# Kernel optimization log

Measured on AMD Instinct MI355X. Metric: run time of the kernel, lower is better.

Reference implementation:

```python
import jax, jax.numpy as jnp
import numpy as np

D_MODEL = 1024
N_LAYER = 4
D_INNER = 2048   # expand * d_model
D_STATE = 16
D_CONV = 4
DT_RANK = 64     # ceil(d_model / 16)
B, L = 2, 1024
EPS = 1e-5


def setup_inputs() -> dict:
    key = jax.random.key(0)
    ks = jax.random.split(key, 10)
    nl = N_LAYER
    def nrm(k, shape, s=0.02):
        return jax.random.normal(k, shape, jnp.float32) * s
    A_log = jnp.broadcast_to(jnp.log(jnp.arange(1, D_STATE + 1, dtype=jnp.float32)),
                             (nl, D_INNER, D_STATE)) + jnp.zeros((nl, D_INNER, D_STATE), jnp.float32)
    return {
        "hidden_states": jax.random.normal(ks[0], (B, L, D_MODEL), jnp.float32),
        "in_proj_w": nrm(ks[1], (nl, 2 * D_INNER, D_MODEL)),
        "conv_w": nrm(ks[2], (nl, D_INNER, D_CONV), 0.1),
        "conv_b": nrm(ks[3], (nl, D_INNER), 0.02),
        "x_proj_w": nrm(ks[4], (nl, DT_RANK + 2 * D_STATE, D_INNER)),
        "dt_proj_w": nrm(ks[5], (nl, D_INNER, DT_RANK), DT_RANK ** -0.5),
        "dt_proj_b": jnp.log(jnp.expm1(jax.random.uniform(ks[6], (nl, D_INNER), jnp.float32, 1e-3, 0.1))),
        "A_log": A_log,
        "D": jnp.ones((nl, D_INNER), jnp.float32),
        "out_proj_w": nrm(ks[7], (nl, D_MODEL, D_INNER)),
        "norm_w": jnp.ones((nl, D_MODEL), jnp.float32),
        "norm_b": jnp.zeros((nl, D_MODEL), jnp.float32),
        "normf_w": jnp.ones((D_MODEL,), jnp.float32),
        "normf_b": jnp.zeros((D_MODEL,), jnp.float32),
    }


def _layernorm(x, w, b):
    mu = x.mean(-1, keepdims=True)
    var = ((x - mu) ** 2).mean(-1, keepdims=True)
    return (x - mu) * jax.lax.rsqrt(var + EPS) * w + b


def _mamba(h, iw, cw, cb, xw, dw, db, Alog, Dp, ow):
    Bn, Ln, _ = h.shape
    xz = jnp.einsum('bld,ed->ble', h, iw)          # [B,L,2*d_inner]
    x, z = jnp.split(xz, 2, axis=-1)
    # depthwise causal conv1d over time, kernel size D_CONV
    xp = jnp.pad(x, ((0, 0), (D_CONV - 1, 0), (0, 0)))
    xc = sum(xp[:, k:k + Ln, :] * cw[:, k] for k in range(D_CONV)) + cb
    x = jax.nn.silu(xc)
    dbl = jnp.einsum('bld,ed->ble', x, xw)         # [B,L,dt_rank+2*d_state]
    dt = dbl[..., :DT_RANK]
    Bm = dbl[..., DT_RANK:DT_RANK + D_STATE]
    Cm = dbl[..., DT_RANK + D_STATE:]
    dt = jax.nn.softplus(jnp.einsum('blr,dr->bld', dt, dw) + db)  # [B,L,d_inner]
    A = -jnp.exp(Alog)                              # [d_inner,d_state]

    def step(hc, inp):
        dt_t, B_t, C_t, x_t = inp                   # [B,d],[B,s],[B,s],[B,d]
        dA = jnp.exp(dt_t[:, :, None] * A)
        hc = hc * dA + (dt_t * x_t)[:, :, None] * B_t[:, None, :]
        y_t = jnp.einsum('bds,bs->bd', hc, C_t)
        return hc, y_t

    h0 = jnp.zeros((Bn, D_INNER, D_STATE), x.dtype)
    xs = (dt.transpose(1, 0, 2), Bm.transpose(1, 0, 2),
          Cm.transpose(1, 0, 2), x.transpose(1, 0, 2))
    _, ys = jax.lax.scan(step, h0, xs)              # ys: [L,B,d_inner]
    y = ys.transpose(1, 0, 2) + x * Dp
    y = y * jax.nn.silu(z)
    return jnp.einsum('bld,ed->ble', y, ow)


def reference(hidden_states, in_proj_w, conv_w, conv_b, x_proj_w, dt_proj_w,
              dt_proj_b, A_log, D, out_proj_w, norm_w, norm_b, normf_w, normf_b):
    hs = hidden_states
    residual = None
    for i in range(N_LAYER):
        residual = hs if residual is None else hs + residual
        hs = _layernorm(residual, norm_w[i], norm_b[i])
        hs = _mamba(hs, in_proj_w[i], conv_w[i], conv_b[i], x_proj_w[i],
                    dt_proj_w[i], dt_proj_b[i], A_log[i], D[i], out_proj_w[i])
    residual = hs + residual
    return _layernorm(residual, normf_w, normf_b)
```

## Files before the change

kernel.cpp:

```cpp
#include <hip/hip_runtime.h>
#include <math.h>

#define D_MODEL 1024
#define D_INNER 2048
#define D_STATE 16
#define D_CONV  4
#define DT_RANK 64
#define NB      2
#define LSEQ    1024
#define NROWS   (NB * LSEQ)
#define LN_EPS  1e-5f
#define N_LAYER 4
#define NCHUNK  32
#define TCH     (LSEQ / NCHUNK)

__device__ inline unsigned bfbits(float f) {
    unsigned u = __float_as_uint(f);
    return (u + 0x7fffu + ((u >> 16) & 1u)) >> 16;
}

#define GLOAD_LDS16(gp, lp) \
    __builtin_amdgcn_global_load_lds( \
        (const __attribute__((address_space(1))) void*)(gp), \
        (__attribute__((address_space(3))) void*)(lp), 16, 0, 0)

__device__ inline float wave_sum(float s) {
    #pragma unroll
    for (int m = 1; m < 64; m <<= 1) s += __shfl_xor(s, m, 64);
    return s;
}

__device__ inline void add_ln_body(int row, int tid,
                                   const float* __restrict__ add,
                                   float* __restrict__ residual,
                                   const float* __restrict__ w, const float* __restrict__ b,
                                   void* __restrict__ out, int first, int bf16out,
                                   float* red)
{
    size_t base = (size_t)row * D_MODEL + tid * 4;

    float4 v = *(const float4*)(add + base);
    if (!first) {
        float4 r = *(const float4*)(residual + base);
        v.x += r.x; v.y += r.y; v.z += r.z; v.w += r.w;
    }
    *(float4*)(residual + base) = v;

    float s = v.x + v.y + v.z + v.w;
    s = wave_sum(s);
    if ((tid & 63) == 0) red[tid >> 6] = s;
    __syncthreads();
    float mu = (red[0] + red[1] + red[2] + red[3]) * (1.0f / D_MODEL);

    float dx = v.x - mu, dy = v.y - mu, dz = v.z - mu, dw2 = v.w - mu;
    float s2 = dx*dx + dy*dy + dz*dz + dw2*dw2;
    s2 = wave_sum(s2);
    if ((tid & 63) == 0) red[4 + (tid >> 6)] = s2;
    __syncthreads();
    float var = (red[4] + red[5] + red[6] + red[7]) * (1.0f / D_MODEL);
    float rs = rsqrtf(var + LN_EPS);

    float4 wv = *(const float4*)(w + tid * 4);
    float4 bv = *(const float4*)(b + tid * 4);
    float4 o;
    o.x = dx  * rs * wv.x + bv.x;
    o.y = dy  * rs * wv.y + bv.y;
    o.z = dz  * rs * wv.z + bv.z;
    o.w = dw2 * rs * wv.w + bv.w;
    if (bf16out) {
        ushort4 ov;
        ov.x = (unsigned short)bfbits(o.x);
        ov.y = (unsigned short)bfbits(o.y);
        ov.z = (unsigned short)bfbits(o.z);
        ov.w = (unsigned short)bfbits(o.w);
        *(ushort4*)((unsigned short*)out + base) = ov;
    } else {
        *(float4*)((float*)out + base) = o;
    }
}

__global__ __launch_bounds__(256)
void add_ln_kernel(const float* __restrict__ add, float* __restrict__ residual,
                   const float* __restrict__ w, const float* __restrict__ b,
                   void* __restrict__ out, int first, int bf16out)
{
    __shared__ float red[8];
    add_ln_body(blockIdx.x, threadIdx.x, add, residual, w, b, out, first, bf16out, red);
}

__global__ __launch_bounds__(256)
void f32_to_bf16_kernel(const float* __restrict__ src, unsigned short* __restrict__ dst)
{
    int i = blockIdx.x * 256 + threadIdx.x;
    float4 v = *(const float4*)(src + (size_t)i * 4);
    ushort4 o;
    o.x = (unsigned short)bfbits(v.x);
    o.y = (unsigned short)bfbits(v.y);
    o.z = (unsigned short)bfbits(v.z);
    o.w = (unsigned short)bfbits(v.w);
    *(ushort4*)(dst + (size_t)i * 4) = o;
}

__device__ inline void hl_split4(float4 v, ushort4* h4, ushort4* l4)
{
    ushort4 h, l;
    float f;
    h.x = (unsigned short)bfbits(v.x); f = __uint_as_float((unsigned)h.x << 16); l.x = (unsigned short)bfbits(v.x - f);
    h.y = (unsigned short)bfbits(v.y); f = __uint_as_float((unsigned)h.y << 16); l.y = (unsigned short)bfbits(v.y - f);
    h.z = (unsigned short)bfbits(v.z); f = __uint_as_float((unsigned)h.z << 16); l.z = (unsigned short)bfbits(v.z - f);
    h.w = (unsigned short)bfbits(v.w); f = __uint_as_float((unsigned)h.w << 16); l.w = (unsigned short)bfbits(v.w - f);
    *h4 = h; *l4 = l;
}

__global__ __launch_bounds__(256)
void lnprep_kernel(const float* __restrict__ add, float* __restrict__ residual,
                   const float* __restrict__ w, const float* __restrict__ b,
                   unsigned short* __restrict__ ln_out, int first,
                   const float* __restrict__ iw, unsigned short* __restrict__ wbuf_in,
                   const float* __restrict__ xw, unsigned short* __restrict__ xwh,
                   unsigned short* __restrict__ xwl,
                   const float* __restrict__ dw, unsigned short* __restrict__ dwh,
                   unsigned short* __restrict__ dwl,
                   float* __restrict__ dbl)
{
    __shared__ float red[8];
    int b0 = blockIdx.x;
    int tid = threadIdx.x;
    if (b0 < 2048) {
        add_ln_body(b0, tid, add, residual, w, b, ln_out, first, 1, red);
    } else if (b0 < 6144) {
        int i = (b0 - 2048) * 256 + tid;
        float4 v = *(const float4*)(iw + (size_t)i * 4);
        ushort4 o;
        o.x = (unsigned short)bfbits(v.x);
        o.y = (unsigned short)bfbits(v.y);
        o.z = (unsigned short)bfbits(v.z);
        o.w = (unsigned short)bfbits(v.w);
        *(ushort4*)(wbuf_in + (size_t)i * 4) = o;
    } else if (b0 < 6336) {
        int i = (b0 - 6144) * 256 + tid;
        float4 v = *(const float4*)(xw + (size_t)i * 4);
        hl_split4(v, (ushort4*)(xwh + (size_t)i * 4), (ushort4*)(xwl + (size_t)i * 4));
    } else if (b0 < 6464) {
        int i = (b0 - 6336) * 256 + tid;
        float4 v = *(const float4*)(dw + (size_t)i * 4);
        hl_split4(v, (ushort4*)(dwh + (size_t)i * 4), (ushort4*)(dwl + (size_t)i * 4));
    } else {
        int i = (b0 - 6464) * 256 + tid;
        *(float4*)(dbl + (size_t)i * 4) = make_float4(0.f, 0.f, 0.f, 0.f);
    }
}

using bf16x8 = __attribute__((ext_vector_type(8))) short;
using f32x4  = __attribute__((ext_vector_type(4))) float;

#define BBM 128
#define BBN 128
#define BBK 64

__global__ __launch_bounds__(256)
void gemm_bf16_nt(const unsigned short* __restrict__ A, const unsigned short* __restrict__ Bw,
                  float* __restrict__ C, int M, int N, int K)
{
    __shared__ unsigned short As[BBM * BBK];
    __shared__ unsigned short Bs[BBN * BBK];

    int tid = threadIdx.x;
    int m0 = blockIdx.y * BBM, n0 = blockIdx.x * BBN;
    int lane = tid & 63, w = tid >> 6;
    int wm = (w >> 1) * 64, wn = (w & 1) * 64;
    int lm = lane & 15, q = lane >> 4;

    int lrow8 = lane >> 3;
    int scol  = ((lane & 7) ^ lrow8) * 8;

    f32x4 acc[4][4] = {};

    for (int k0 = 0; k0 < K; k0 += BBK) {
        #pragma unroll
        for (int j = 0; j < 4; ++j) {
            int rbase = w * 32 + j * 8;
            GLOAD_LDS16(A + (size_t)(m0 + rbase + lrow8) * K + k0 + scol,
                        &As[rbase * BBK]);
        }
        #pragma unroll
        for (int j = 0; j < 4; ++j) {
            int rbase = w * 32 + j * 8;
            GLOAD_LDS16(Bw + (size_t)(n0 + rbase + lrow8) * K + k0 + scol,
                        &Bs[rbase * BBK]);
        }
        __syncthreads();
        #pragma unroll
        for (int kk = 0; kk < BBK; kk += 32) {
            bf16x8 af[4], bf[4];
            #pragma unroll
            for (int i = 0; i < 4; ++i) {
                int row = wm + i * 16 + lm;
                int col = (kk + q * 8) ^ ((row & 7) << 3);
                af[i] = *(const bf16x8*)&As[row * BBK + col];
            }
            #pragma unroll
            for (int j = 0; j < 4; ++j) {
                int row = wn + j * 16 + lm;
                int col = (kk + q * 8) ^ ((row & 7) << 3);
                bf[j] = *(const bf16x8*)&Bs[row * BBK + col];
            }
            #pragma unroll
            for (int i = 0; i < 4; ++i)
                #pragma unroll
                for (int j = 0; j < 4; ++j)
                    acc[i][j] = __builtin_amdgcn_mfma_f32_16x16x32_bf16(
                        af[i], bf[j], acc[i][j], 0, 0, 0);
        }
        __syncthreads();
    }

    #pragma unroll
    for (int i = 0; i < 4; ++i)
        #pragma unroll
        for (int j = 0; j < 4; ++j)
            #pragma unroll
            for (int r = 0; r < 4; ++r) {
                int row = m0 + wm + i * 16 + q * 4 + r;
                int col = n0 + wn + j * 16 + lm;
                C[(size_t)row * N + col] = acc[i][j][r];
            }
}

__global__ __launch_bounds__(256)
void xproj_hl(const unsigned short* __restrict__ Ah, const unsigned short* __restrict__ Al,
              const unsigned short* __restrict__ Bh, const unsigned short* __restrict__ Bl,
              float* __restrict__ C)
{
    int tid = threadIdx.x;
    int lane = tid & 63, w = tid >> 6;
    int lm = lane & 15, q = lane >> 4;
    int m0 = blockIdx.x * 32;
    int kb = blockIdx.y * 256;

    int wm = (w & 1) * 16;
    int wn = (w >> 1) * 48;

    size_t arow = (size_t)(m0 + wm + lm) * 2048;

    f32x4 acc[3] = {};

    #pragma unroll 2
    for (int kc = 0; kc < 8; ++kc) {
        int k = kb + kc * 32 + q * 8;
        bf16x8 ah = *(const bf16x8*)&Ah[arow + k];
        bf16x8 al = *(const bf16x8*)&Al[arow + k];
        #pragma unroll
        for (int j = 0; j < 3; ++j) {
            size_t brow = (size_t)(wn + j * 16 + lm) * 2048;
            bf16x8 bh = *(const bf16x8*)&Bh[brow + k];
            bf16x8 bl = *(const bf16x8*)&Bl[brow + k];
            acc[j] = __builtin_amdgcn_mfma_f32_16x16x32_bf16(al, bh, acc[j], 0, 0, 0);
            acc[j] = __builtin_amdgcn_mfma_f32_16x16x32_bf16(ah, bl, acc[j], 0, 0, 0);
            acc[j] = __builtin_amdgcn_mfma_f32_16x16x32_bf16(ah, bh, acc[j], 0, 0, 0);
        }
    }

    #pragma unroll
    for (int j = 0; j < 3; ++j) {
        int col = wn + j * 16 + lm;
        #pragma unroll
        for (int r = 0; r < 4; ++r) {
            int row = m0 + wm + q * 4 + r;
            atomicAdd(&C[(size_t)row * 96 + col], acc[j][r]);
        }
    }
}

__global__ __launch_bounds__(256)
void dtproj_hl(const float* __restrict__ dbl,
               const unsigned short* __restrict__ Bh, const unsigned short* __restrict__ Bl,
               const float* __restrict__ bias, float* __restrict__ dtb)
{
    int tid = threadIdx.x;
    int lane = tid & 63, w = tid >> 6;
    int lm = lane & 15, q = lane >> 4;
    int n0 = blockIdx.x * 128;
    int m0 = blockIdx.y * 64;

    const float* arow = dbl + (size_t)(m0 + w * 16 + lm) * 96;

    f32x4 acc[8] = {};

    #pragma unroll
    for (int kc = 0; kc < 2; ++kc) {
        int k = kc * 32 + q * 8;
        float4 v0 = *(const float4*)(arow + k);
        float4 v1 = *(const float4*)(arow + k + 4);
        float vv[8] = {v0.x, v0.y, v0.z, v0.w, v1.x, v1.y, v1.z, v1.w};
        bf16x8 ah, al;
        #pragma unroll
        for (int s = 0; s < 8; ++s) {
            unsigned hb = bfbits(vv[s]);
            ah[s] = (short)hb;
            al[s] = (short)bfbits(vv[s] - __uint_as_float(hb << 16));
        }
        #pragma unroll
        for (int j = 0; j < 8; ++j) {
            size_t brow = (size_t)(n0 + j * 16 + lm) * 64;
            bf16x8 bh = *(const bf16x8*)&Bh[brow + k];
            bf16x8 bl = *(const bf16x8*)&Bl[brow + k];
            acc[j] = __builtin_amdgcn_mfma_f32_16x16x32_bf16(al, bh, acc[j], 0, 0, 0);
            acc[j] = __builtin_amdgcn_mfma_f32_16x16x32_bf16(ah, bl, acc[j], 0, 0, 0);
            acc[j] = __builtin_amdgcn_mfma_f32_16x16x32_bf16(ah, bh, acc[j], 0, 0, 0);
        }
    }

    #pragma unroll
    for (int j = 0; j < 8; ++j) {
        int col = n0 + j * 16 + lm;
        float bv = bias[col];
        #pragma unroll
        for (int r = 0; r < 4; ++r) {
            int row = m0 + w * 16 + q * 4 + r;
            float v = acc[j][r] + bv;
            v = (v > 20.f) ? v : log1pf(__expf(v));
            dtb[(size_t)row * D_INNER + col] = v;
        }
    }
}

__global__ __launch_bounds__(256)
void conv_silu_kernel(const float* __restrict__ xz, const float* __restrict__ cw,
                      const float* __restrict__ cb, float* __restrict__ xc,
                      unsigned short* __restrict__ xch, unsigned short* __restrict__ xcl)
{
    int idx = blockIdx.x * 256 + threadIdx.x;
    int d  = idx & (D_INNER - 1);
    int t  = (idx >> 11) & (LSEQ - 1);
    int bb = idx >> 21;

    const float* xcol = xz + (size_t)bb * LSEQ * 2 * D_INNER + d;
    float acc = cb[d];
    #pragma unroll
    for (int k = 0; k < D_CONV; ++k) {
        int tt = t + k - (D_CONV - 1);
        if (tt >= 0) acc += xcol[(size_t)tt * 2 * D_INNER] * cw[d * D_CONV + k];
    }
    acc = acc / (1.f + __expf(-acc));
    xc[idx] = acc;
    unsigned hb = bfbits(acc);
    xch[idx] = (unsigned short)hb;
    float hf = __uint_as_float(hb << 16);
    xcl[idx] = (unsigned short)bfbits(acc - hf);
}

#define UNPK4(dst, off, v) { dst[(off)+0]=(v).x; dst[(off)+1]=(v).y; \
                             dst[(off)+2]=(v).z; dst[(off)+3]=(v).w; }

__global__ __launch_bounds__(256)
void scan_pass1(const float* __restrict__ dtb, const float* __restrict__ xc,
                const float* __restrict__ dbl, const float* __restrict__ Alog,
                float* __restrict__ aPbuf, float* __restrict__ bAbuf)
{
    int tid  = threadIdx.x;
    int half = tid & 1;
    int blk  = blockIdx.x;
    int dg   = blk & 15;
    int c    = (blk >> 4) & (NCHUNK - 1);
    int bb   = blk >> 9;
    int d    = dg * 128 + (tid >> 1);

    float A[8];
    {
        const float* pA = Alog + (size_t)d * D_STATE + half * 8;
        float4 v0 = *(const float4*)pA;
        float4 v1 = *(const float4*)(pA + 4);
        A[0] = -__expf(v0.x); A[1] = -__expf(v0.y);
        A[2] = -__expf(v0.z); A[3] = -__expf(v0.w);
        A[4] = -__expf(v1.x); A[5] = -__expf(v1.y);
        A[6] = -__expf(v1.z); A[7] = -__expf(v1.w);
    }

    size_t rowbase = (size_t)bb * LSEQ + (size_t)c * TCH;
    const float* pdt = dtb + rowbase * D_INNER + d;
    const float* pxc = xc  + rowbase * D_INNER + d;
    const float* pbc = dbl + rowbase * 96 + DT_RANK + half * 8;

    float aP[8] = {1.f,1.f,1.f,1.f,1.f,1.f,1.f,1.f};
    float bA[8] = {0.f,0.f,0.f,0.f,0.f,0.f,0.f,0.f};

    float  dtE = pdt[0], xvE = pxc[0];
    float4 BE0 = *(const float4*)pbc;
    float4 BE1 = *(const float4*)(pbc + 4);
    float  dtO = pdt[D_INNER], xvO = pxc[D_INNER];
    float4 BO0 = *(const float4*)(pbc + 96);
    float4 BO1 = *(const float4*)(pbc + 96 + 4);

    const float* qdtE = pdt + 2 * D_INNER;
    const float* qdtO = pdt + 3 * D_INNER;
    const float* qxcE = pxc + 2 * D_INNER;
    const float* qxcO = pxc + 3 * D_INNER;
    const float* qbcE = pbc + 2 * 96;
    const float* qbcO = pbc + 3 * 96;

#define P1_STEP(DT, XV, B0, B1) { \
        float B[8]; UNPK4(B, 0, B0) UNPK4(B, 4, B1) \
        float dtx = (DT) * (XV); \
        _Pragma("unroll") \
        for (int s = 0; s < 8; ++s) { \
            float a = __expf((DT) * A[s]); \
            aP[s] *= a; \
            bA[s] = bA[s] * a + dtx * B[s]; \
        } }

    for (int t = 0; t < TCH - 4; t += 2) {
        float  dtEn = qdtE[0], xvEn = qxcE[0];
        float4 BE0n = *(const float4*)qbcE;
        float4 BE1n = *(const float4*)(qbcE + 4);
        float  dtOn = qdtO[0], xvOn = qxcO[0];
        float4 BO0n = *(const float4*)qbcO;
        float4 BO1n = *(const float4*)(qbcO + 4);
        qdtE += 2 * D_INNER; qdtO += 2 * D_INNER;
        qxcE += 2 * D_INNER; qxcO += 2 * D_INNER;
        qbcE += 192; qbcO += 192;

        P1_STEP(dtE, xvE, BE0, BE1)
        P1_STEP(dtO, xvO, BO0, BO1)

        dtE = dtEn; xvE = xvEn; BE0 = BE0n; BE1 = BE1n;
        dtO = dtOn; xvO = xvOn; BO0 = BO0n; BO1 = BO1n;
    }
    {
        float  dtEn = qdtE[0], xvEn = qxcE[0];
        float4 BE0n = *(const float4*)qbcE;
        float4 BE1n = *(const float4*)(qbcE + 4);
        float  dtOn = qdtO[0], xvOn = qxcO[0];
        float4 BO0n = *(const float4*)qbcO;
        float4 BO1n = *(const float4*)(qbcO + 4);

        P1_STEP(dtE, xvE, BE0, BE1)
        P1_STEP(dtO, xvO, BO0, BO1)

        dtE = dtEn; xvE = xvEn; BE0 = BE0n; BE1 = BE1n;
        dtO = dtOn; xvO = xvOn; BO0 = BO0n; BO1 = BO1n;
    }
    {
        P1_STEP(dtE, xvE, BE0, BE1)
        P1_STEP(dtO, xvO, BO0, BO1)
    }
#undef P1_STEP

    float* pa = aPbuf + ((size_t)(bb * NCHUNK + c) * D_INNER + d) * D_STATE + half * 8;
    float* pb = bAbuf + ((size_t)(bb * NCHUNK + c) * D_INNER + d) * D_STATE + half * 8;
    *(float4*)(pa + 0) = make_float4(aP[0], aP[1], aP[2], aP[3]);
    *(float4*)(pa + 4) = make_float4(aP[4], aP[5], aP[6], aP[7]);
    *(float4*)(pb + 0) = make_float4(bA[0], bA[1], bA[2], bA[3]);
    *(float4*)(pb + 4) = make_float4(bA[4], bA[5], bA[6], bA[7]);
}

__global__ __launch_bounds__(256)
void scan_pass2(const float* __restrict__ dtb, const float* __restrict__ xc,
                const float* __restrict__ dbl, const float* __restrict__ xz,
                const float* __restrict__ Alog, const float* __restrict__ Dp,
                const float* __restrict__ aPbuf, const float* __restrict__ bAbuf,
                unsigned short* __restrict__ y)
{
    int tid  = threadIdx.x;
    int half = tid & 1;
    int blk  = blockIdx.x;
    int dg   = blk & 15;
    int c    = (blk >> 4) & (NCHUNK - 1);
    int bb   = blk >> 9;
    int d    = dg * 128 + (tid >> 1);

    float A[8];
    {
        const float* pA = Alog + (size_t)d * D_STATE + half * 8;
        float4 v0 = *(const float4*)pA;
        float4 v1 = *(const float4*)(pA + 4);
        A[0] = -__expf(v0.x); A[1] = -__expf(v0.y);
        A[2] = -__expf(v0.z); A[3] = -__expf(v0.w);
        A[4] = -__expf(v1.x); A[5] = -__expf(v1.y);
        A[6] = -__expf(v1.z); A[7] = -__expf(v1.w);
    }
    float Dd = Dp[d];

    float h[8] = {0.f,0.f,0.f,0.f,0.f,0.f,0.f,0.f};

    for (int cc = 0; cc < c; ++cc) {
        const float* pa = aPbuf + ((size_t)(bb * NCHUNK + cc) * D_INNER + d) * D_STATE + half * 8;
        const float* pb = bAbuf + ((size_t)(bb * NCHUNK + cc) * D_INNER + d) * D_STATE + half * 8;
        float4 a0 = *(const float4*)(pa + 0), a1 = *(const float4*)(pa + 4);
        float4 b0 = *(const float4*)(pb + 0), b1 = *(const float4*)(pb + 4);
        float av[8], bv[8];
        UNPK4(av, 0, a0) UNPK4(av, 4, a1)
        UNPK4(bv, 0, b0) UNPK4(bv, 4, b1)
        #pragma unroll
        for (int s = 0; s < 8; ++s) h[s] = h[s] * av[s] + bv[s];
    }

    size_t rowbase = (size_t)bb * LSEQ + (size_t)c * TCH;
    const float* pdt = dtb + rowbase * D_INNER + d;
    const float* pxc = xc  + rowbase * D_INNER + d;
    const float* pz  = xz  + rowbase * 2 * D_INNER + D_INNER + d;
    const float* pbc = dbl + rowbase * 96 + DT_RANK + half * 8;
    unsigned short* qyE = y + rowbase * D_INNER + d;
    unsigned short* qyO = qyE + D_INNER;

    float  dtE = pdt[0], xvE = pxc[0], zvE = pz[0];
    float4 BE0 = *(const float4*)pbc;
    float4 BE1 = *(const float4*)(pbc + 4);
    float4 CE0 = *(const float4*)(pbc + 16);
    float4 CE1 = *(const float4*)(pbc + 20);
    float  dtO = pdt[D_INNER], xvO = pxc[D_INNER], zvO = pz[2 * D_INNER];
    float4 BO0 = *(const float4*)(pbc + 96);
    float4 BO1 = *(const float4*)(pbc + 96 + 4);
    float4 CO0 = *(const float4*)(pbc + 96 + 16);
    float4 CO1 = *(const float4*)(pbc + 96 + 20);

    const float* qdtE = pdt + 2 * D_INNER;
    const float* qdtO = pdt + 3 * D_INNER;
    const float* qxcE = pxc + 2 * D_INNER;
    const float* qxcO = pxc + 3 * D_INNER;
    const float* qzE  = pz  + 4 * D_INNER;
    const float* qzO  = pz  + 6 * D_INNER;
    const float* qbcE = pbc + 2 * 96;
    const float* qbcO = pbc + 3 * 96;

#define P2_STEP(DT, XV, ZV, B0, B1, C0, C1, PY) { \
        float B[8], C[8]; \
        UNPK4(B, 0, B0) UNPK4(B, 4, B1) \
        UNPK4(C, 0, C0) UNPK4(C, 4, C1) \
        float dtx = (DT) * (XV); \
        float p = 0.f; \
        _Pragma("unroll") \
        for (int s = 0; s < 8; ++s) { \
            float a = __expf((DT) * A[s]); \
            h[s] = h[s] * a + dtx * B[s]; \
            p += h[s] * C[s]; \
        } \
        p += __shfl_xor(p, 1, 2); \
        if (half == 0) { \
            float sz = (ZV) / (1.f + __expf(-(ZV))); \
            *(PY) = (unsigned short)bfbits((p + (XV) * Dd) * sz); \
        } }

    for (int t = 0; t < TCH - 4; t += 2) {
        float  dtEn = qdtE[0], xvEn = qxcE[0], zvEn = qzE[0];
        float4 BE0n = *(const float4*)qbcE;
        float4 BE1n = *(const float4*)(qbcE + 4);
        float4 CE0n = *(const float4*)(qbcE + 16);
        float4 CE1n = *(const float4*)(qbcE + 20);
        float  dtOn = qdtO[0], xvOn = qxcO[0], zvOn = qzO[0];
        float4 BO0n = *(const float4*)qbcO;
        float4 BO1n = *(const float4*)(qbcO + 4);
        float4 CO0n = *(const float4*)(qbcO + 16);
        float4 CO1n = *(const float4*)(qbcO + 20);
        qdtE += 2 * D_INNER; qdtO += 2 * D_INNER;
        qxcE += 2 * D_INNER; qxcO += 2 * D_INNER;
        qzE  += 4 * D_INNER; qzO  += 4 * D_INNER;
        qbcE += 192; qbcO += 192;

        P2_STEP(dtE, xvE, zvE, BE0, BE1, CE0, CE1, qyE)
        qyE += 2 * D_INNER;
        P2_STEP(dtO, xvO, zvO, BO0, BO1, CO0, CO1, qyO)
        qyO += 2 * D_INNER;

        dtE = dtEn; xvE = xvEn; zvE = zvEn;
        BE0 = BE0n; BE1 = BE1n; CE0 = CE0n; CE1 = CE1n;
        dtO = dtOn; xvO = xvOn; zvO = zvOn;
        BO0 = BO0n; BO1 = BO1n; CO0 = CO0n; CO1 = CO1n;
    }
    {
        float  dtEn = qdtE[0], xvEn = qxcE[0], zvEn = qzE[0];
        float4 BE0n = *(const float4*)qbcE;
        float4 BE1n = *(const float4*)(qbcE + 4);
        float4 CE0n = *(const float4*)(qbcE + 16);
        float4 CE1n = *(const float4*)(qbcE + 20);
        float  dtOn = qdtO[0], xvOn = qxcO[0], zvOn = qzO[0];
        float4 BO0n = *(const float4*)qbcO;
        float4 BO1n = *(const float4*)(qbcO + 4);
        float4 CO0n = *(const float4*)(qbcO + 16);
        float4 CO1n = *(const float4*)(qbcO + 20);

        P2_STEP(dtE, xvE, zvE, BE0, BE1, CE0, CE1, qyE)
        qyE += 2 * D_INNER;
        P2_STEP(dtO, xvO, zvO, BO0, BO1, CO0, CO1, qyO)
        qyO += 2 * D_INNER;

        dtE = dtEn; xvE = xvEn; zvE = zvEn;
        BE0 = BE0n; BE1 = BE1n; CE0 = CE0n; CE1 = CE1n;
        dtO = dtOn; xvO = xvOn; zvO = zvOn;
        BO0 = BO0n; BO1 = BO1n; CO0 = CO0n; CO1 = CO1n;
    }
    {
        P2_STEP(dtE, xvE, zvE, BE0, BE1, CE0, CE1, qyE)
        P2_STEP(dtO, xvO, zvO, BO0, BO1, CO0, CO1, qyO)
    }
#undef P2_STEP
}

extern "C" void kernel_launch(void* const* d_in, const int* in_sizes, int n_in,
                              void* d_out, int out_size, void* d_ws, size_t ws_size,
                              hipStream_t stream)
{
    const float* h_in  = (const float*)d_in[0];
    const float* iw    = (const float*)d_in[1];
    const float* cw    = (const float*)d_in[2];
    const float* cb    = (const float*)d_in[3];
    const float* xw    = (const float*)d_in[4];
    const float* dw    = (const float*)d_in[5];
    const float* db    = (const float*)d_in[6];
    const float* Alog  = (const float*)d_in[7];
    const float* Dp    = (const float*)d_in[8];
    const float* ow    = (const float*)d_in[9];
    const float* nw    = (const float*)d_in[10];
    const float* nb    = (const float*)d_in[11];
    const float* nfw   = (const float*)d_in[12];
    const float* nfb   = (const float*)d_in[13];

    float* ws = (float*)d_ws;
    float* residual = ws;
    float* hs       = residual + 2097152;
    float* xz       = hs + 2097152;
    float* xc       = xz + 8388608;
    float* dtb      = xc + 4194304;
    float* dbl      = dtb + 4194304;
    float* y        = dbl + 196608;

    float* aPbuf = hs;
    float* bAbuf = y + 2097152;

    unsigned short* wbuf_in  = (unsigned short*)y;
    unsigned short* hs_bf16  = (unsigned short*)(y + 2097152);
    unsigned short* y_bf16   = (unsigned short*)y;
    unsigned short* xc_hi    = (unsigned short*)y;
    unsigned short* xc_lo    = (unsigned short*)(y + 2097152);
    unsigned short* xwp_hi   = (unsigned short*)hs;
    unsigned short* xwp_lo   = (unsigned short*)(hs + 98304);
    unsigned short* dwp_hi   = (unsigned short*)(hs + 196608);
    unsigned short* dwp_lo   = (unsigned short*)(hs + 262144);
    unsigned short* wbuf_out = (unsigned short*)dtb;

    const float* cur_add = h_in;
    for (int i = 0; i < N_LAYER; ++i) {
        lnprep_kernel<<<6656, 256, 0, stream>>>(
            cur_add, residual, nw + i * D_MODEL, nb + i * D_MODEL, hs_bf16, i == 0,
            iw + (size_t)i * 2 * D_INNER * D_MODEL, wbuf_in,
            xw + (size_t)i * 96 * D_INNER, xwp_hi, xwp_lo,
            dw + (size_t)i * D_INNER * DT_RANK, dwp_hi, dwp_lo,
            dbl);
        gemm_bf16_nt<<<dim3(2 * D_INNER / BBN, NROWS / BBM), 256, 0, stream>>>(
            hs_bf16, wbuf_in, xz, NROWS, 2 * D_INNER, D_MODEL);
        conv_silu_kernel<<<NB * LSEQ * D_INNER / 256, 256, 0, stream>>>(
            xz, cw + (size_t)i * D_INNER * D_CONV, cb + i * D_INNER, xc, xc_hi, xc_lo);
        xproj_hl<<<dim3(NROWS / 32, 8), 256, 0, stream>>>(
            xc_hi, xc_lo, xwp_hi, xwp_lo, dbl);
        dtproj_hl<<<dim3(D_INNER / 128, NROWS / 64), 256, 0, stream>>>(
            dbl, dwp_hi, dwp_lo, db + i * D_INNER, dtb);
        scan_pass1<<<NB * NCHUNK * (D_INNER / 128), 256, 0, stream>>>(
            dtb, xc, dbl, Alog + (size_t)i * D_INNER * D_STATE, aPbuf, bAbuf);
        scan_pass2<<<NB * NCHUNK * (D_INNER / 128), 256, 0, stream>>>(
            dtb, xc, dbl, xz, Alog + (size_t)i * D_INNER * D_STATE, Dp + i * D_INNER,
            aPbuf, bAbuf, y_bf16);
        f32_to_bf16_kernel<<<(D_MODEL * D_INNER) / 1024, 256, 0, stream>>>(
            ow + (size_t)i * D_MODEL * D_INNER, wbuf_out);
        gemm_bf16_nt<<<dim3(D_MODEL / BBN, NROWS / BBM), 256, 0, stream>>>(
            y_bf16, wbuf_out, hs, NROWS, D_MODEL, D_INNER);
        cur_add = hs;
    }
    add_ln_kernel<<<NROWS, 256, 0, stream>>>(hs, residual, nfw, nfb, d_out, 0, 0);
}
```

Measured before the change: 961.3 us.

## Add separate chunk-prefix scan kernel to replace redundant per-block prefix in pass2

Adds a scan_prefix kernel that walks the chunk summaries (decay products and accumulated inputs) sequentially per (batch, channel, state pair) and writes each chunk's incoming state in place into bAbuf. scan_pass2 then loads its initial state with one read instead of replaying all previous chunks, which removed the quadratic O(NCHUNK^2) re-reads of aPbuf/bAbuf. The cost is one extra kernel launch per layer and a short serial 32-step loop, with less parallelism in that step.

```diff
diff --git a/kernel.cpp b/kernel.cpp
--- a/kernel.cpp
+++ b/kernel.cpp
@@ -455,10 +455,32 @@
 }
 
 __global__ __launch_bounds__(256)
+void scan_prefix(const float* __restrict__ aPbuf, float* __restrict__ bAbuf)
+{
+    int idx = blockIdx.x * 256 + threadIdx.x;
+    int sp = idx & 7;
+    int d  = (idx >> 3) & (D_INNER - 1);
+    int bb = idx >> 14;
+
+    size_t o = ((size_t)(bb * NCHUNK) * D_INNER + d) * D_STATE + sp * 2;
+    const size_t stride = (size_t)D_INNER * D_STATE;
+    float h0 = 0.f, h1 = 0.f;
+    #pragma unroll 4
+    for (int c = 0; c < NCHUNK; ++c) {
+        float2 a2 = *(const float2*)(aPbuf + o);
+        float2 b2 = *(const float2*)(bAbuf + o);
+        *(float2*)(bAbuf + o) = make_float2(h0, h1);
+        h0 = h0 * a2.x + b2.x;
+        h1 = h1 * a2.y + b2.y;
+        o += stride;
+    }
+}
+
+__global__ __launch_bounds__(256)
 void scan_pass2(const float* __restrict__ dtb, const float* __restrict__ xc,
                 const float* __restrict__ dbl, const float* __restrict__ xz,
                 const float* __restrict__ Alog, const float* __restrict__ Dp,
-                const float* __restrict__ aPbuf, const float* __restrict__ bAbuf,
+                const float* __restrict__ bAbuf,
                 unsigned short* __restrict__ y)
 {
     int tid  = threadIdx.x;
@@ -481,18 +503,12 @@
     }
     float Dd = Dp[d];
 
-    float h[8] = {0.f,0.f,0.f,0.f,0.f,0.f,0.f,0.f};
-
-    for (int cc = 0; cc < c; ++cc) {
-        const float* pa = aPbuf + ((size_t)(bb * NCHUNK + cc) * D_INNER + d) * D_STATE + half * 8;
-        const float* pb = bAbuf + ((size_t)(bb * NCHUNK + cc) * D_INNER + d) * D_STATE + half * 8;
-        float4 a0 = *(const float4*)(pa + 0), a1 = *(const float4*)(pa + 4);
-        float4 b0 = *(const float4*)(pb + 0), b1 = *(const float4*)(pb + 4);
-        float av[8], bv[8];
-        UNPK4(av, 0, a0) UNPK4(av, 4, a1)
-        UNPK4(bv, 0, b0) UNPK4(bv, 4, b1)
-        #pragma unroll
-        for (int s = 0; s < 8; ++s) h[s] = h[s] * av[s] + bv[s];
+    float h[8];
+    {
+        const float* ph = bAbuf + ((size_t)(bb * NCHUNK + c) * D_INNER + d) * D_STATE + half * 8;
+        float4 h0v = *(const float4*)(ph + 0);
+        float4 h1v = *(const float4*)(ph + 4);
+        UNPK4(h, 0, h0v) UNPK4(h, 4, h1v)
     }
 
     size_t rowbase = (size_t)bb * LSEQ + (size_t)c * TCH;
@@ -656,9 +672,10 @@
             dbl, dwp_hi, dwp_lo, db + i * D_INNER, dtb);
         scan_pass1<<<NB * NCHUNK * (D_INNER / 128), 256, 0, stream>>>(
             dtb, xc, dbl, Alog + (size_t)i * D_INNER * D_STATE, aPbuf, bAbuf);
+        scan_prefix<<<(NB * D_INNER * 8) / 256, 256, 0, stream>>>(aPbuf, bAbuf);
         scan_pass2<<<NB * NCHUNK * (D_INNER / 128), 256, 0, stream>>>(
             dtb, xc, dbl, xz, Alog + (size_t)i * D_INNER * D_STATE, Dp + i * D_INNER,
-            aPbuf, bAbuf, y_bf16);
+            bAbuf, y_bf16);
         f32_to_bf16_kernel<<<(D_MODEL * D_INNER) / 1024, 256, 0, stream>>>(
             ow + (size_t)i * D_MODEL * D_INNER, wbuf_out);
         gemm_bf16_nt<<<dim3(D_MODEL / BBN, NROWS / BBM), 256, 0, stream>>>(
```

Result: faster. 942.2 us (-2.0%).
